# Kernel tuning notes

Measured on AMD Instinct MI355X. Metric: run time of the kernel, lower is better.

## Reference

```python
import jax, jax.numpy as jnp
import numpy as np
from jax import lax

B, N, C = 16, 131072, 3
NPOINT = 1024
OUT = 384
HID = OUT // 2


def farthest_point_sample(points, npoint):
    """points: [B, N, 3] -> idx: [B, npoint] int32 (classic FPS, start at index 0)."""
    b, n, _ = points.shape

    def body(carry, _):
        min_dist, last_idx = carry
        last = jnp.take_along_axis(points, last_idx[:, None, None], axis=1)  # [B,1,3]
        d = jnp.sum((points - last) ** 2, axis=-1)                           # [B,N]
        min_dist = jnp.minimum(min_dist, d)
        nxt = jnp.argmax(min_dist, axis=-1).astype(jnp.int32)
        return (min_dist, nxt), nxt

    idx0 = jnp.zeros((b,), jnp.int32)
    dist0 = jnp.full((b, n), 1e10, dtype=points.dtype)
    _, idxs = lax.scan(body, (dist0, idx0), None, length=npoint - 1)  # [npoint-1, B]
    return jnp.concatenate([idx0[None, :], idxs], axis=0).T           # [B, npoint]


def shared_mlp(x, w1, b1, w2, b2):
    # Conv1d(kernel_size=1) == pointwise linear; x: [B, M, Cin]
    h = jax.nn.gelu(jnp.einsum('bmc,ch->bmh', x, w1) + b1, approximate=False)
    return jnp.einsum('bmh,ho->bmo', h, w2) + b2


def setup_inputs() -> dict:
    key = jax.random.key(0)
    ks = jax.random.split(key, 9)
    points = jax.random.normal(ks[0], (B, N, C), dtype=jnp.float32)
    s1 = 1.0 / np.sqrt(C)
    s2 = 1.0 / np.sqrt(HID)
    return {
        'points': points,
        'w1t': jax.random.uniform(ks[1], (C, HID), jnp.float32, -s1, s1),
        'b1t': jax.random.uniform(ks[2], (HID,), jnp.float32, -s1, s1),
        'w2t': jax.random.uniform(ks[3], (HID, OUT), jnp.float32, -s2, s2),
        'b2t': jax.random.uniform(ks[4], (OUT,), jnp.float32, -s2, s2),
        'w1p': jax.random.uniform(ks[5], (C, HID), jnp.float32, -s1, s1),
        'b1p': jax.random.uniform(ks[6], (HID,), jnp.float32, -s1, s1),
        'w2p': jax.random.uniform(ks[7], (HID, OUT), jnp.float32, -s2, s2),
        'b2p': jax.random.uniform(ks[8], (OUT,), jnp.float32, -s2, s2),
    }


def reference(points, w1t, b1t, w2t, b2t, w1p, b1p, w2p, b2p):
    center_idx = farthest_point_sample(points, NPOINT)                      # [B, npoint]
    center = jnp.take_along_axis(points, center_idx[:, :, None], axis=1)   # [B, npoint, 3]
    det_token = shared_mlp(center, w1t, b1t, w2t, b2t)                      # [B, npoint, OUT]
    det_pos = shared_mlp(center, w1p, b1p, w2p, b2p)                        # [B, npoint, OUT]
    return det_token, det_pos
```

## Files before the change

### kernel.cpp

```cpp
#include <hip/hip_runtime.h>

#define NB 16
#define NPTS 131072
#define NPOINT 1024
#define HID 192
#define OUTC 384
#define BLKS_PER_B 16
#define THREADS_FPS 1024
#define PTS_PER_T (NPTS / BLKS_PER_B / THREADS_FPS)
#define TAG_INIT 1023u

__global__ __launch_bounds__(1024) void fps_kernel(
    const float* __restrict__ points,
    unsigned long long* __restrict__ slots,
    int* __restrict__ fps_idx)
{
  const int blk = blockIdx.x;
  const int b = blk >> 4;
  const int r = blk & 15;
  const int t = threadIdx.x;
  const float* __restrict__ P = points + (size_t)b * NPTS * 3;
  const int base = r * (NPTS / BLKS_PER_B);

  float px[PTS_PER_T], py[PTS_PER_T], pz[PTS_PER_T], md[PTS_PER_T];
  unsigned int lowk[PTS_PER_T];
#pragma unroll
  for (int k = 0; k < PTS_PER_T; ++k) {
    int i = base + (k << 10) + t;
    const float* pp = P + (size_t)i * 3;
    px[k] = pp[0]; py[k] = pp[1]; pz[k] = pp[2];
    md[k] = 1e10f;
    lowk[k] = 0xFFFFFFFFu - (unsigned int)i;
  }

  float lx = P[0], ly = P[1], lz = P[2];

  __shared__ unsigned long long s_red[16];
  __shared__ int s_nidx;

  unsigned long long* slot_b = slots + b * 32;

  for (int it = 0; it < NPOINT - 1; ++it) {
    unsigned long long best = 0ull;
#pragma unroll
    for (int k = 0; k < PTS_PER_T; ++k) {
      float dx = px[k] - lx;
      float dy = py[k] - ly;
      float dz = pz[k] - lz;
      float d = __fadd_rn(__fadd_rn(__fmul_rn(dx, dx), __fmul_rn(dy, dy)), __fmul_rn(dz, dz));
      float m = fminf(md[k], d);
      md[k] = m;
      unsigned long long key =
          ((unsigned long long)__float_as_uint(m) << 32) | (unsigned long long)lowk[k];
      best = key > best ? key : best;
    }
#pragma unroll
    for (int off = 32; off > 0; off >>= 1) {
      unsigned int lo = (unsigned int)best, hi = (unsigned int)(best >> 32);
      lo = __shfl_down(lo, off, 64);
      hi = __shfl_down(hi, off, 64);
      unsigned long long o = ((unsigned long long)hi << 32) | (unsigned long long)lo;
      best = o > best ? o : best;
    }
    const int lane = t & 63, wid = t >> 6;
    if (lane == 0) s_red[wid] = best;
    __syncthreads();
    if (t < 16) {
      unsigned long long v = s_red[t];
#pragma unroll
      for (int off = 8; off > 0; off >>= 1) {
        unsigned int lo = (unsigned int)v, hi = (unsigned int)(v >> 32);
        lo = __shfl_xor(lo, off, 64);
        hi = __shfl_xor(hi, off, 64);
        unsigned long long o = ((unsigned long long)hi << 32) | (unsigned long long)lo;
        v = o > v ? o : v;
      }
      unsigned long long* buf = slot_b + ((it & 1) << 4);
      if (t == 0) {
        unsigned int i = 0xFFFFFFFFu - (unsigned int)v;
        unsigned long long inv17 = (unsigned long long)((NPTS - 1) - i);
        unsigned long long sv = (v & 0xFFFFFFFF00000000ull) | (inv17 << 15) |
                                (unsigned long long)(unsigned int)it;
        __hip_atomic_store(&buf[r], sv, __ATOMIC_RELAXED, __HIP_MEMORY_SCOPE_AGENT);
      }
      unsigned long long pv;
      do {
        pv = __hip_atomic_load(&buf[t], __ATOMIC_RELAXED, __HIP_MEMORY_SCOPE_AGENT);
      } while ((unsigned int)(pv & 0x3FFull) != (unsigned int)it);
#pragma unroll
      for (int off = 8; off > 0; off >>= 1) {
        unsigned int lo = (unsigned int)pv, hi = (unsigned int)(pv >> 32);
        lo = __shfl_xor(lo, off, 64);
        hi = __shfl_xor(hi, off, 64);
        unsigned long long o = ((unsigned long long)hi << 32) | (unsigned long long)lo;
        pv = o > pv ? o : pv;
      }
      if (t == 0) {
        int nidx = (int)(NPTS - 1) - (int)((pv >> 15) & 0x1FFFFull);
        s_nidx = nidx;
        if (r == 0) fps_idx[b * NPOINT + it + 1] = nidx;
      }
    }
    __syncthreads();
    int nidx = s_nidx;
    const float* lp = P + (size_t)nidx * 3;
    lx = lp[0]; ly = lp[1]; lz = lp[2];
  }
}

__global__ void fps_init_kernel(unsigned long long* __restrict__ slots,
                                int* __restrict__ fps_idx)
{
  int i = blockIdx.x * blockDim.x + threadIdx.x;
  if (i < NB * 2 * 16) slots[i] = (unsigned long long)TAG_INIT;
  if (i < NB) fps_idx[i * NPOINT] = 0;
}

__global__ __launch_bounds__(384) void mlp_kernel(
    const float* __restrict__ points,
    const int* __restrict__ fps_idx,
    const float* __restrict__ w1t, const float* __restrict__ b1t,
    const float* __restrict__ w2t, const float* __restrict__ b2t,
    const float* __restrict__ w1p, const float* __restrict__ b1p,
    const float* __restrict__ w2p, const float* __restrict__ b2p,
    float* __restrict__ out)
{
  __shared__ float s_c[4][3];
  __shared__ float s_h[2][HID][4];
  const int t = threadIdx.x;
  const int m0 = blockIdx.x * 4;
  if (t < 4) {
    int m = m0 + t;
    int b = m >> 10;
    int idx = fps_idx[m];
    const float* p = points + ((size_t)b * NPTS + (size_t)idx) * 3;
    s_c[t][0] = p[0]; s_c[t][1] = p[1]; s_c[t][2] = p[2];
  }
  __syncthreads();
  {
    const int mlp = t / HID;
    const int k = t - mlp * HID;
    const float* w1 = mlp ? w1p : w1t;
    const float* b1 = mlp ? b1p : b1t;
    float wa = w1[k], wb = w1[HID + k], wc = w1[2 * HID + k], bb = b1[k];
#pragma unroll
    for (int r = 0; r < 4; ++r) {
      float z = s_c[r][0] * wa + s_c[r][1] * wb + s_c[r][2] * wc + bb;
      float g = 0.5f * z * (1.0f + erff(z * 0.70710678118654752440f));
      s_h[mlp][k][r] = g;
    }
  }
  __syncthreads();
  const int o = t;
  float acct[4] = {0.f, 0.f, 0.f, 0.f};
  float accp[4] = {0.f, 0.f, 0.f, 0.f};
  const float* w2t_o = w2t + o;
  const float* w2p_o = w2p + o;
#pragma unroll 4
  for (int k = 0; k < HID; ++k) {
    float wt = w2t_o[(size_t)k * OUTC];
    float wp = w2p_o[(size_t)k * OUTC];
    float4 ht = *(const float4*)&s_h[0][k][0];
    float4 hp = *(const float4*)&s_h[1][k][0];
    acct[0] = fmaf(ht.x, wt, acct[0]);
    acct[1] = fmaf(ht.y, wt, acct[1]);
    acct[2] = fmaf(ht.z, wt, acct[2]);
    acct[3] = fmaf(ht.w, wt, acct[3]);
    accp[0] = fmaf(hp.x, wp, accp[0]);
    accp[1] = fmaf(hp.y, wp, accp[1]);
    accp[2] = fmaf(hp.z, wp, accp[2]);
    accp[3] = fmaf(hp.w, wp, accp[3]);
  }
  float bt = b2t[o], bp = b2p[o];
  const size_t posoff = (size_t)NB * NPOINT * OUTC;
#pragma unroll
  for (int rr = 0; rr < 4; ++rr) {
    size_t m = (size_t)(m0 + rr);
    out[m * OUTC + o] = acct[rr] + bt;
    out[posoff + m * OUTC + o] = accp[rr] + bp;
  }
}

extern "C" void kernel_launch(void* const* d_in, const int* in_sizes, int n_in,
                              void* d_out, int out_size, void* d_ws, size_t ws_size,
                              hipStream_t stream)
{
  const float* points = (const float*)d_in[0];
  const float* w1t = (const float*)d_in[1];
  const float* b1t = (const float*)d_in[2];
  const float* w2t = (const float*)d_in[3];
  const float* b2t = (const float*)d_in[4];
  const float* w1p = (const float*)d_in[5];
  const float* b1p = (const float*)d_in[6];
  const float* w2p = (const float*)d_in[7];
  const float* b2p = (const float*)d_in[8];
  float* out = (float*)d_out;

  char* ws = (char*)d_ws;
  unsigned long long* slots = (unsigned long long*)(ws + 0);
  int* fps_idx = (int*)(ws + 4096);

  hipLaunchKernelGGL(fps_init_kernel, dim3(2), dim3(256), 0, stream,
                     slots, fps_idx);

  void* args[3];
  args[0] = (void*)&points;
  args[1] = (void*)&slots;
  args[2] = (void*)&fps_idx;
  hipLaunchCooperativeKernel((void*)fps_kernel, dim3(NB * BLKS_PER_B),
                             dim3(THREADS_FPS), args, 0, stream);

  hipLaunchKernelGGL(mlp_kernel, dim3(NB * NPOINT / 4), dim3(384), 0, stream,
                     points, fps_idx, w1t, b1t, w2t, b2t, w1p, b1p, w2p, b2p, out);
}
```

Measured before the change: 2.529 ms.

## Exchange winner coordinates through slots to drop per-iteration global point reload

```diff
diff --git a/kernel.cpp b/kernel.cpp
--- a/kernel.cpp
+++ b/kernel.cpp
@@ -7,8 +7,16 @@
 #define OUTC 384
 #define BLKS_PER_B 16
 #define THREADS_FPS 1024
-#define PTS_PER_T (NPTS / BLKS_PER_B / THREADS_FPS)
+#define PTS_PER_T 8
 #define TAG_INIT 1023u
+#define SLOT_U64 16
+
+__device__ __forceinline__ unsigned long long shfl_u64(unsigned long long v, int src) {
+  unsigned int lo = (unsigned int)v, hi = (unsigned int)(v >> 32);
+  lo = __shfl(lo, src, 64);
+  hi = __shfl(hi, src, 64);
+  return ((unsigned long long)hi << 32) | lo;
+}
 
 __global__ __launch_bounds__(1024) void fps_kernel(
     const float* __restrict__ points,
@@ -19,92 +27,132 @@
   const int b = blk >> 4;
   const int r = blk & 15;
   const int t = threadIdx.x;
+  const int lane = t & 63, wid = t >> 6;
   const float* __restrict__ P = points + (size_t)b * NPTS * 3;
-  const int base = r * (NPTS / BLKS_PER_B);
+  const int base = r << 13;
 
   float px[PTS_PER_T], py[PTS_PER_T], pz[PTS_PER_T], md[PTS_PER_T];
-  unsigned int lowk[PTS_PER_T];
 #pragma unroll
   for (int k = 0; k < PTS_PER_T; ++k) {
     int i = base + (k << 10) + t;
     const float* pp = P + (size_t)i * 3;
     px[k] = pp[0]; py[k] = pp[1]; pz[k] = pp[2];
     md[k] = 1e10f;
-    lowk[k] = 0xFFFFFFFFu - (unsigned int)i;
   }
 
   float lx = P[0], ly = P[1], lz = P[2];
 
-  __shared__ unsigned long long s_red[16];
-  __shared__ int s_nidx;
-
-  unsigned long long* slot_b = slots + b * 32;
+  __shared__ unsigned long long s_key[2][16];
+  __shared__ float s_x[2][16], s_y[2][16], s_z[2][16];
+
+  unsigned long long* slot_b = slots + (size_t)b * 2 * 16 * SLOT_U64;
 
   for (int it = 0; it < NPOINT - 1; ++it) {
-    unsigned long long best = 0ull;
+    const int par = it & 1;
+    float bm = -1.0f; int bk = 0;
 #pragma unroll
     for (int k = 0; k < PTS_PER_T; ++k) {
-      float dx = px[k] - lx;
-      float dy = py[k] - ly;
-      float dz = pz[k] - lz;
+      float dx = px[k] - lx, dy = py[k] - ly, dz = pz[k] - lz;
       float d = __fadd_rn(__fadd_rn(__fmul_rn(dx, dx), __fmul_rn(dy, dy)), __fmul_rn(dz, dz));
       float m = fminf(md[k], d);
       md[k] = m;
-      unsigned long long key =
-          ((unsigned long long)__float_as_uint(m) << 32) | (unsigned long long)lowk[k];
-      best = key > best ? key : best;
-    }
+      if (m > bm) { bm = m; bk = k; }
+    }
+    int bi = base + (bk << 10) + t;
+    unsigned long long key = ((unsigned long long)__float_as_uint(bm) << 32)
+                           | ((unsigned long long)(unsigned)(NPTS - 1 - bi) << 15);
 #pragma unroll
     for (int off = 32; off > 0; off >>= 1) {
-      unsigned int lo = (unsigned int)best, hi = (unsigned int)(best >> 32);
+      unsigned int lo = (unsigned int)key, hi = (unsigned int)(key >> 32);
       lo = __shfl_down(lo, off, 64);
       hi = __shfl_down(hi, off, 64);
-      unsigned long long o = ((unsigned long long)hi << 32) | (unsigned long long)lo;
-      best = o > best ? o : best;
-    }
-    const int lane = t & 63, wid = t >> 6;
-    if (lane == 0) s_red[wid] = best;
+      unsigned long long o = ((unsigned long long)hi << 32) | lo;
+      key = o > key ? o : key;
+    }
+    key = shfl_u64(key, 0);
+    {
+      int iw = NPTS - 1 - (int)((key >> 15) & 0x1FFFFull);
+      int tw = (iw - base) & 1023;
+      int kw = (iw - base) >> 10;
+      float xc = px[0], yc = py[0], zc = pz[0];
+#pragma unroll
+      for (int k = 1; k < PTS_PER_T; ++k) {
+        bool s = (kw == k);
+        xc = s ? px[k] : xc; yc = s ? py[k] : yc; zc = s ? pz[k] : zc;
+      }
+      float xw = __shfl(xc, tw & 63, 64);
+      float yw = __shfl(yc, tw & 63, 64);
+      float zw = __shfl(zc, tw & 63, 64);
+      if (lane == 0) {
+        s_key[par][wid] = key;
+        s_x[par][wid] = xw; s_y[par][wid] = yw; s_z[par][wid] = zw;
+      }
+    }
     __syncthreads();
-    if (t < 16) {
-      unsigned long long v = s_red[t];
+    unsigned long long bkey = 0ull;
+    if (lane < 16) {
+      bkey = s_key[par][lane];
 #pragma unroll
       for (int off = 8; off > 0; off >>= 1) {
-        unsigned int lo = (unsigned int)v, hi = (unsigned int)(v >> 32);
+        unsigned int lo = (unsigned int)bkey, hi = (unsigned int)(bkey >> 32);
         lo = __shfl_xor(lo, off, 64);
         hi = __shfl_xor(hi, off, 64);
-        unsigned long long o = ((unsigned long long)hi << 32) | (unsigned long long)lo;
-        v = o > v ? o : v;
-      }
-      unsigned long long* buf = slot_b + ((it & 1) << 4);
-      if (t == 0) {
-        unsigned int i = 0xFFFFFFFFu - (unsigned int)v;
-        unsigned long long inv17 = (unsigned long long)((NPTS - 1) - i);
-        unsigned long long sv = (v & 0xFFFFFFFF00000000ull) | (inv17 << 15) |
-                                (unsigned long long)(unsigned int)it;
-        __hip_atomic_store(&buf[r], sv, __ATOMIC_RELAXED, __HIP_MEMORY_SCOPE_AGENT);
-      }
-      unsigned long long pv;
-      do {
-        pv = __hip_atomic_load(&buf[t], __ATOMIC_RELAXED, __HIP_MEMORY_SCOPE_AGENT);
-      } while ((unsigned int)(pv & 0x3FFull) != (unsigned int)it);
+        unsigned long long o = ((unsigned long long)hi << 32) | lo;
+        bkey = o > bkey ? o : bkey;
+      }
+    }
+    bkey = shfl_u64(bkey, 0);
+    int ib = NPTS - 1 - (int)((bkey >> 15) & 0x1FFFFull);
+    int wb = ((ib - base) & 1023) >> 6;
+    unsigned long long* buf = slot_b + (size_t)par * 16 * SLOT_U64;
+    if (t == 0) {
+      float bx = s_x[par][wb], by = s_y[par][wb], bz = s_z[par][wb];
+      unsigned long long tg = (unsigned long long)(unsigned int)it;
+      unsigned long long* sl = buf + (size_t)r * SLOT_U64;
+      __hip_atomic_store(&sl[1], ((unsigned long long)__float_as_uint(bx) << 32) | tg,
+                         __ATOMIC_RELAXED, __HIP_MEMORY_SCOPE_AGENT);
+      __hip_atomic_store(&sl[2], ((unsigned long long)__float_as_uint(by) << 32) | tg,
+                         __ATOMIC_RELAXED, __HIP_MEMORY_SCOPE_AGENT);
+      __hip_atomic_store(&sl[3], ((unsigned long long)__float_as_uint(bz) << 32) | tg,
+                         __ATOMIC_RELAXED, __HIP_MEMORY_SCOPE_AGENT);
+      __hip_atomic_store(&sl[0], bkey | tg,
+                         __ATOMIC_RELAXED, __HIP_MEMORY_SCOPE_AGENT);
+    }
+    unsigned long long g0 = 0ull; float fx = 0.f, fy = 0.f, fz = 0.f;
+    if (lane < 16) {
+      unsigned long long* sl = buf + (size_t)lane * SLOT_U64;
+      unsigned long long g1, g2, g3;
+      const unsigned int uit = (unsigned int)it;
+      for (;;) {
+        g0 = __hip_atomic_load(&sl[0], __ATOMIC_RELAXED, __HIP_MEMORY_SCOPE_AGENT);
+        g1 = __hip_atomic_load(&sl[1], __ATOMIC_RELAXED, __HIP_MEMORY_SCOPE_AGENT);
+        g2 = __hip_atomic_load(&sl[2], __ATOMIC_RELAXED, __HIP_MEMORY_SCOPE_AGENT);
+        g3 = __hip_atomic_load(&sl[3], __ATOMIC_RELAXED, __HIP_MEMORY_SCOPE_AGENT);
+        unsigned int bad = (((unsigned int)g0 & 0x3FFu) ^ uit)
+                         | (((unsigned int)g1 & 0x3FFu) ^ uit)
+                         | (((unsigned int)g2 & 0x3FFu) ^ uit)
+                         | (((unsigned int)g3 & 0x3FFu) ^ uit);
+        if (!bad) break;
+      }
+      fx = __uint_as_float((unsigned int)(g1 >> 32));
+      fy = __uint_as_float((unsigned int)(g2 >> 32));
+      fz = __uint_as_float((unsigned int)(g3 >> 32));
 #pragma unroll
       for (int off = 8; off > 0; off >>= 1) {
-        unsigned int lo = (unsigned int)pv, hi = (unsigned int)(pv >> 32);
+        unsigned int lo = (unsigned int)g0, hi = (unsigned int)(g0 >> 32);
         lo = __shfl_xor(lo, off, 64);
         hi = __shfl_xor(hi, off, 64);
-        unsigned long long o = ((unsigned long long)hi << 32) | (unsigned long long)lo;
-        pv = o > pv ? o : pv;
-      }
-      if (t == 0) {
-        int nidx = (int)(NPTS - 1) - (int)((pv >> 15) & 0x1FFFFull);
-        s_nidx = nidx;
-        if (r == 0) fps_idx[b * NPOINT + it + 1] = nidx;
-      }
-    }
-    __syncthreads();
-    int nidx = s_nidx;
-    const float* lp = P + (size_t)nidx * 3;
-    lx = lp[0]; ly = lp[1]; lz = lp[2];
+        unsigned long long o = ((unsigned long long)hi << 32) | lo;
+        g0 = o > g0 ? o : g0;
+      }
+    }
+    g0 = shfl_u64(g0, 0);
+    int gi = NPTS - 1 - (int)((g0 >> 15) & 0x1FFFFull);
+    int gr = gi >> 13;
+    lx = __shfl(fx, gr, 64);
+    ly = __shfl(fy, gr, 64);
+    lz = __shfl(fz, gr, 64);
+    if (r == 0 && t == 0) fps_idx[b * NPOINT + it + 1] = gi;
   }
 }
 
@@ -112,7 +160,7 @@
                                 int* __restrict__ fps_idx)
 {
   int i = blockIdx.x * blockDim.x + threadIdx.x;
-  if (i < NB * 2 * 16) slots[i] = (unsigned long long)TAG_INIT;
+  if (i < NB * 2 * 16 * SLOT_U64) slots[i] = (unsigned long long)TAG_INIT;
   if (i < NB) fps_idx[i * NPOINT] = 0;
 }
 
@@ -198,9 +246,9 @@
 
   char* ws = (char*)d_ws;
   unsigned long long* slots = (unsigned long long*)(ws + 0);
-  int* fps_idx = (int*)(ws + 4096);
-
-  hipLaunchKernelGGL(fps_init_kernel, dim3(2), dim3(256), 0, stream,
+  int* fps_idx = (int*)(ws + 65536);
+
+  hipLaunchKernelGGL(fps_init_kernel, dim3(32), dim3(256), 0, stream,
                      slots, fps_idx);
 
   void* args[3];
```

Result: slower. 7.649 ms (+202.5%).
